# Optimization experiments

Hardware: AMD Instinct MI355X
Metric: run time of the kernel (lower is better)

The kernel has to match this reference:

```python
import jax, jax.numpy as jnp
import numpy as np

IN_NC = 32
OUT_NC = 32
EXPAND = 2
HID = IN_NC * EXPAND          # 64
K = 3                         # depthwise kernel
EPS = 1e-5
R1 = IN_NC * HID              # end of pointwise-1 weights
R2 = R1 + HID * K * K         # end of depthwise weights
R3 = R2 + HID * OUT_NC        # total hyper params = 4672


def _bn(t, g, b):
    # BatchNorm2d in training mode over the flattened (b*fh*fw) batch:
    # stats over all axes except the channel axis (axis=3 of [b,fh,fw,C,H,W]).
    ax = (0, 1, 2, 4, 5)
    m = jnp.mean(t, axis=ax, keepdims=True)
    v = jnp.mean((t - m) ** 2, axis=ax, keepdims=True)
    sh = (1, 1, 1, -1, 1, 1)
    return (t - m) * jax.lax.rsqrt(v + EPS) * g.reshape(sh) + b.reshape(sh)


def _relu6(t):
    return jnp.clip(t, 0.0, 6.0)


def setup_inputs() -> dict:
    key = jax.random.key(0)
    k0, k1 = jax.random.split(key)
    x = jax.random.normal(k0, (8, IN_NC, 256, 256), dtype=jnp.float32)
    s = jax.random.normal(k1, (8, R3, 32, 32), dtype=jnp.float32) * 0.1
    return {
        'x': x,
        's': s,
        'gamma1': jnp.ones((HID,), jnp.float32),
        'beta1': jnp.zeros((HID,), jnp.float32),
        'gamma2': jnp.ones((HID,), jnp.float32),
        'beta2': jnp.zeros((HID,), jnp.float32),
        'gamma3': jnp.ones((OUT_NC,), jnp.float32),
        'beta3': jnp.zeros((OUT_NC,), jnp.float32),
    }


def reference(x, s, gamma1, beta1, gamma2, beta2, gamma3, beta3):
    b, c, h, w = x.shape
    fh, fw = s.shape[-2], s.shape[-1]
    ph, pw = h // fh, w // fw          # patch size
    kh, kw = ph + 2, pw + 2            # patch + reflect halo of 1

    # reflect-pad then extract overlapping [kh,kw] patches on a [ph,pw] grid
    xp = jnp.pad(x, ((0, 0), (0, 0), (1, 1), (1, 1)), mode='reflect')
    ri = (jnp.arange(fh) * ph)[:, None] + jnp.arange(kh)   # [fh,kh]
    ci = (jnp.arange(fw) * pw)[:, None] + jnp.arange(kw)   # [fw,kw]
    patches = xp[:, :, ri][:, :, :, :, ci]                 # [b,c,fh,kh,fw,kw]
    patches = patches.transpose(0, 2, 4, 1, 3, 5)          # [b,fh,fw,c,kh,kw]

    sw = s.transpose(0, 2, 3, 1)                           # [b,fh,fw,R3]

    # stage 1: per-patch 1x1 expand conv (in_nc -> hidden)
    w1 = sw[..., :R1].reshape(b, fh, fw, HID, c)
    y = jnp.einsum('bfgoc,bfgchw->bfgohw', w1, patches)    # [b,fh,fw,HID,kh,kw]
    y = _relu6(_bn(y, gamma1, beta1))

    # stage 2: per-patch depthwise 3x3 conv (valid), stride 1 -> [ph,pw]
    w2 = sw[..., R1:R2].reshape(b, fh, fw, HID, K, K)
    z = jnp.zeros((b, fh, fw, HID, ph, pw), y.dtype)
    for u in range(K):
        for v in range(K):
            z = z + w2[..., u, v, None, None] * y[..., u:u + ph, v:v + pw]
    z = _relu6(_bn(z, gamma2, beta2))

    # stage 3: per-patch 1x1 project conv (hidden -> out_nc)
    w3 = sw[..., R2:R3].reshape(b, fh, fw, OUT_NC, HID)
    o = jnp.einsum('bfgoc,bfgcpq->bfgopq', w3, z)          # [b,fh,fw,OUT_NC,ph,pw]
    o = _bn(o, gamma3, beta3)

    # reassemble patches: [b,fh,fw,C,ph,pw] -> [b,C,h,w]
    o = o.transpose(0, 3, 1, 4, 2, 5).reshape(b, OUT_NC, h, w)
    return x + o  # use_res_connect: stride==1 and in_nc==out_nc
```

## Files before the change

kernel.cpp:

```cpp
#include <hip/hip_runtime.h>

#define NT 256

constexpr int R1c = 2048;
constexpr int R2c = 2624;
constexpr float EPSc = 1e-5f;

constexpr int SLOTS1  = 0;
constexpr int SLOTS1Q = 4096;
constexpr int SLOTS2  = 8192;
constexpr int SLOTS2Q = 12288;
constexpr int SLOTS3  = 16384;
constexpr int SLOTS3Q = 18432;
constexpr int STATS_ZERO_FLOATS = 20480;

constexpr size_t ST2_OFF   = 131072;
constexpr size_t ST2_BYTES = 8ull * 1024 * 4672 * 2;
constexpr size_t ZB_OFF    = ST2_OFF + ST2_BYTES;
constexpr size_t ZB_BYTES  = 8192ull * 4096 * 2;
constexpr size_t Y_OFF     = ZB_OFF + ZB_BYTES;
constexpr size_t Y_BYTES   = 8192ull * 13312;
constexpr size_t NEED_Y    = Y_OFF + Y_BYTES;
constexpr size_t OI_OFF    = Y_OFF;

__device__ __forceinline__ ushort f_to_bf16(float f) {
    union { float f; unsigned int i; } v; v.f = f;
    unsigned int r = (v.i + 0x7fffu + ((v.i >> 16) & 1u)) >> 16;
    return (ushort)r;
}
__device__ __forceinline__ float bf16_to_f(ushort u) {
    union { unsigned int i; float f; } v; v.i = ((unsigned int)u) << 16; return v.f;
}
__device__ __forceinline__ float bf16lo_to_f(unsigned int u) {
    union { unsigned int i; float f; } v; v.i = u << 16; return v.f;
}
__device__ __forceinline__ float bf16hi_to_f(unsigned int u) {
    union { unsigned int i; float f; } v; v.i = u & 0xffff0000u; return v.f;
}
__device__ __forceinline__ unsigned int pack_bf16(float lo, float hi) {
    return (unsigned int)f_to_bf16(lo) | ((unsigned int)f_to_bf16(hi) << 16);
}

typedef short bf16x8 __attribute__((ext_vector_type(8)));
typedef float f32x4  __attribute__((ext_vector_type(4)));
union FR { uint4 u4; bf16x8 v; ushort s[8]; };

__device__ __forceinline__ f32x4 mfma16(bf16x8 a, bf16x8 b, f32x4 c) {
    return __builtin_amdgcn_mfma_f32_16x16x32_bf16(a, b, c, 0, 0, 0);
}

__device__ __forceinline__ void dev_fin(const float* __restrict__ ws, int so, int sq,
        const float* __restrict__ gamma, const float* __restrict__ beta,
        int nch, float N, float* finL, int t) {
    if (t < nch) {
        float sm = 0.f, qq = 0.f;
        for (int j = 0; j < 64; j++) { sm += ws[so + t*64 + j]; qq += ws[sq + t*64 + j]; }
        float mean = sm / N;
        float var  = qq / N - mean * mean;
        float a = rsqrtf(var + EPSc) * gamma[t];
        finL[t]       = a;
        finL[nch + t] = beta[t] - mean * a;
    }
    __syncthreads();
}

__global__ __launch_bounds__(256)
void transpose_w(const float* __restrict__ s, ushort* __restrict__ st,
                 float* __restrict__ ws) {
    __shared__ float tl[2112];
    const int tile = blockIdx.x, t = threadIdx.x;
    if (tile < 80) {
        int idx = tile * 256 + t;
        if (idx < STATS_ZERO_FLOATS) ws[idx] = 0.f;
    }
    const int bi = tile / (73 * 32);
    int rem = tile - bi * 73 * 32;
    const int qy = rem / 73, px = rem - qy * 73;
    const int p0 = px * 64, q0 = qy * 32;
    const int tx = t & 31, ty = t >> 5;
    const float* sb = s + (size_t)bi * 4672 * 1024;
    #pragma unroll
    for (int r = ty; r < 64; r += 8)
        tl[r * 33 + tx] = sb[(size_t)(p0 + r) * 1024 + q0 + tx];
    __syncthreads();
    unsigned int* stu = (unsigned int*)(st + (size_t)bi * 1024 * 4672);
    #pragma unroll
    for (int rr = ty; rr < 32; rr += 8) {
        int q = q0 + rr;
        stu[((size_t)q * 4672 + p0) / 2 + tx] =
            pack_bf16(tl[(2 * tx) * 33 + rr], tl[(2 * tx + 1) * 33 + rr]);
    }
}

__global__ __launch_bounds__(NT, 4)
void k1_w(const float* __restrict__ x, const ushort* __restrict__ st2,
          ushort* __restrict__ ybuf, float* __restrict__ ws) {
    __shared__ __align__(16) ushort frB[2 * 3584];
    __shared__ float st1[128];
    const int t = threadIdx.x, unit = blockIdx.x;
    const int bi = unit >> 9, f = (unit >> 4) & 31, jb = unit & 15;
    const int g0 = jb * 2, slot = unit & 63;
    const int w = t >> 6, l = t & 63, l15 = l & 15, grp = l >> 4;
    const int pl_ = w >> 1, mh = w & 1;
    const int patch = bi * 1024 + f * 32 + g0 + pl_;

    if (t < 128) {
        st1[t] = 0.f;
        int p = t >> 6, e = t & 63;
        if ((e & 15) >= 4)
            ((uint4*)frB)[p * 448 + 384 + e] = make_uint4(0u, 0u, 0u, 0u);
    }
    const ushort* wp = st2 + (size_t)patch * 4672;
    FR aw[2];
    #pragma unroll
    for (int i = 0; i < 2; i++)
        aw[i].u4 = ((const uint4*)wp)[((mh * 2 + i) * 16 + l15) * 4 + grp];

    const float* xb = x + (size_t)bi * 32 * 65536;
    for (int i = t; i < 1920; i += NT) {
        int c = i / 60, rem = i - c * 60;
        int r = rem / 6, seg = rem - r * 6;
        int row = f * 8 - 1 + r; row = row < 0 ? -row : (row > 255 ? 510 - row : row);
        int col0 = g0 * 8 - 4 + seg * 4;
        float v4[4];
        if (col0 >= 0 && col0 <= 252) {
            float4 vv = *(const float4*)(xb + (size_t)c * 65536 + row * 256 + col0);
            v4[0] = vv.x; v4[1] = vv.y; v4[2] = vv.z; v4[3] = vv.w;
        } else {
            #pragma unroll
            for (int d = 0; d < 4; d++) {
                int cc = col0 + d; cc = cc < 0 ? -cc : (cc > 255 ? 510 - cc : cc);
                v4[d] = xb[(size_t)c * 65536 + row * 256 + cc];
            }
        }
        int grpc = c >> 3, j = c & 7;
        #pragma unroll
        for (int d = 0; d < 4; d++) {
            int u = col0 + d - g0 * 8;
            ushort hv = f_to_bf16(v4[d]);
            #pragma unroll
            for (int p = 0; p < 2; p++) {
                int pc = u - 8 * p + 1;
                if (pc >= 0 && pc <= 9) {
                    int px = r * 10 + pc;
                    frB[p * 3584 + ((px >> 4) * 64 + grpc * 16 + (px & 15)) * 8 + j] = hv;
                }
            }
        }
    }
    __syncthreads();

    FR b[7];
    const uint4* bp = (const uint4*)(frB + pl_ * 3584);
    #pragma unroll
    for (int n = 0; n < 7; n++) b[n].u4 = bp[n * 64 + l];
    __syncthreads();

    ushort* slice = frB + pl_ * 3584 + mh * 1792;
    unsigned int* sliceU = (unsigned int*)slice;
    uint4* yb4 = (uint4*)ybuf + (size_t)patch * 832;
    float s4[8], q4[8];
    #pragma unroll
    for (int i = 0; i < 8; i++) { s4[i] = 0.f; q4[i] = 0.f; }
    #pragma unroll
    for (int i = 0; i < 2; i++) {
        int mm = mh * 2 + i;
        #pragma unroll
        for (int n = 0; n < 7; n++) {
            f32x4 z = {0.f, 0.f, 0.f, 0.f};
            f32x4 c = mfma16(aw[i].v, b[n].v, z);
            int px = n * 16 + l15;
            #pragma unroll
            for (int r = 0; r < 4; r++) {
                float v = c[r]; s4[i*4+r] += v; q4[i*4+r] += v * v;
                if (px < 100) slice[(grp * 4 + r) * 106 + px] = f_to_bf16(v);
            }
        }
        for (int k = l; k < 208; k += 64) {
            int ch2 = k / 13, sub = k - ch2 * 13;
            int ub = ch2 * 53 + sub * 4;
            yb4[mm * 208 + k] = make_uint4(sliceU[ub], sliceU[ub+1], sliceU[ub+2], sliceU[ub+3]);
        }
    }
    #pragma unroll
    for (int i = 0; i < 8; i++) {
        float sm = s4[i], qq = q4[i];
        #pragma unroll
        for (int msk = 1; msk <= 8; msk <<= 1) { sm += __shfl_xor(sm, msk); qq += __shfl_xor(qq, msk); }
        if (l15 == 0) {
            int ch = (mh * 2 + (i >> 2)) * 16 + grp * 4 + (i & 3);
            atomicAdd(&st1[ch], sm);
            atomicAdd(&st1[64 + ch], qq);
        }
    }
    __syncthreads();
    if (t < 64) {
        atomicAdd(&ws[SLOTS1  + t * 64 + slot], st1[t]);
        atomicAdd(&ws[SLOTS1Q + t * 64 + slot], st1[64 + t]);
    }
}

__global__ __launch_bounds__(NT, 4)
void k2_w(const ushort* __restrict__ ybuf, const ushort* __restrict__ st2,
          ushort* __restrict__ zbuf, float* __restrict__ ws,
          const float* __restrict__ g1, const float* __restrict__ b1) {
    __shared__ __align__(16) ushort slc[4 * 1696];
    __shared__ unsigned int w2L[2 * 288];
    __shared__ float finL[128];
    __shared__ float accL[128];
    const int t = threadIdx.x, unit = blockIdx.x;
    const int bi = unit >> 9, f = (unit >> 4) & 31, jb = unit & 15;
    const int g0 = jb * 2, slot = unit & 63;
    const int w = t >> 6, l = t & 63;
    const int pl_ = w >> 1, mh = w & 1;
    const int ch_l = l >> 2, quad = l & 3, p0 = quad * 2;
    const int patch = bi * 1024 + f * 32 + g0 + pl_;

    dev_fin(ws, SLOTS1, SLOTS1Q, g1, b1, 64, 819200.0f, finL, t);
    if (t < 128) accL[t] = 0.f;
    for (int k = t; k < 576; k += NT) {
        int p = (k >= 288) ? 1 : 0;
        int kk = k - p * 288;
        const unsigned int* src = (const unsigned int*)(st2 + (size_t)(bi*1024 + f*32 + g0 + p) * 4672 + R1c);
        w2L[k] = src[kk];
    }
    __syncthreads();

    const uint4* yb4 = (const uint4*)ybuf + (size_t)patch * 832;
    ushort* slice = slc + w * 1696;
    unsigned int* sliceU = (unsigned int*)slice;
    const ushort* w2u = (const ushort*)(w2L + pl_ * 288);
    ushort* zp0 = zbuf + (size_t)patch * 4096;

    #pragma unroll
    for (int i = 0; i < 2; i++) {
        int mm = mh * 2 + i;
        for (int k = l; k < 208; k += 64) {
            uint4 v = yb4[mm * 208 + k];
            int ch2 = k / 13, sub = k - ch2 * 13;
            int ch = mm * 16 + ch2;
            float a1 = finL[ch], bb1 = finL[64 + ch];
            unsigned int uu[4] = {v.x, v.y, v.z, v.w};
            int ub = ch2 * 53 + sub * 4;
            #pragma unroll
            for (int kk = 0; kk < 4; kk++) {
                float lo = fminf(fmaxf(bf16lo_to_f(uu[kk]) * a1 + bb1, 0.f), 6.f);
                float hi = fminf(fmaxf(bf16hi_to_f(uu[kk]) * a1 + bb1, 0.f), 6.f);
                sliceU[ub + kk] = pack_bf16(lo, hi);
            }
        }
        float yv[4][10];
        #pragma unroll
        for (int rr = 0; rr < 4; rr++) {
            int base = ch_l * 53 + (p0 + rr) * 5;
            #pragma unroll
            for (int k = 0; k < 5; k++) {
                unsigned int u = sliceU[base + k];
                yv[rr][2*k] = bf16lo_to_f(u); yv[rr][2*k+1] = bf16hi_to_f(u);
            }
        }
        float wt[9];
        #pragma unroll
        for (int k = 0; k < 9; k++) wt[k] = bf16_to_f(w2u[(mm * 16 + ch_l) * 9 + k]);
        float za[2][8];
        #pragma unroll
        for (int rr = 0; rr < 2; rr++)
            #pragma unroll
            for (int q = 0; q < 8; q++) za[rr][q] = 0.f;
        #pragma unroll
        for (int u = 0; u < 3; u++)
            #pragma unroll
            for (int v = 0; v < 3; v++) {
                float wv = wt[u * 3 + v];
                #pragma unroll
                for (int rr = 0; rr < 2; rr++)
                    #pragma unroll
                    for (int q = 0; q < 8; q++)
                        za[rr][q] += wv * yv[rr + u][q + v];
            }
        float zs = 0.f, zq = 0.f;
        #pragma unroll
        for (int rr = 0; rr < 2; rr++)
            #pragma unroll
            for (int q = 0; q < 8; q++) { float v = za[rr][q]; zs += v; zq += v * v; }
        zs += __shfl_xor(zs, 1); zs += __shfl_xor(zs, 2);
        zq += __shfl_xor(zq, 1); zq += __shfl_xor(zq, 2);
        if (quad == 0) {
            atomicAdd(&accL[mm * 16 + ch_l], zs);
            atomicAdd(&accL[64 + mm * 16 + ch_l], zq);
        }
        ushort* zp = zp0 + (mm * 16 + ch_l) * 64 + p0 * 8;
        uint4 pk0, pk1;
        pk0.x = pack_bf16(za[0][0], za[0][1]); pk0.y = pack_bf16(za[0][2], za[0][3]);
        pk0.z = pack_bf16(za[0][4], za[0][5]); pk0.w = pack_bf16(za[0][6], za[0][7]);
        pk1.x = pack_bf16(za[1][0], za[1][1]); pk1.y = pack_bf16(za[1][2], za[1][3]);
        pk1.z = pack_bf16(za[1][4], za[1][5]); pk1.w = pack_bf16(za[1][6], za[1][7]);
        *(uint4*)zp = pk0;
        *(uint4*)(zp + 8) = pk1;
    }
    __syncthreads();
    if (t < 64) {
        atomicAdd(&ws[SLOTS2  + t * 64 + slot], accL[t]);
        atomicAdd(&ws[SLOTS2Q + t * 64 + slot], accL[64 + t]);
    }
}

__global__ __launch_bounds__(NT, 4)
void k3_w(const ushort* __restrict__ zbuf, const ushort* __restrict__ st2,
          ushort* __restrict__ oi, float* __restrict__ ws,
          const float* __restrict__ g2, const float* __restrict__ b2) {
    __shared__ __align__(16) ushort zL[2 * 4224];
    __shared__ float finL[128];
    __shared__ float accL[64];
    const int t = threadIdx.x, unit = blockIdx.x;
    const int bi = unit >> 9, f = (unit >> 4) & 31, jb = unit & 15;
    const int g0 = jb * 2, slot = unit & 63;
    const int w = t >> 6, l = t & 63, l15 = l & 15, grp = l >> 4;
    const int pl_ = w >> 1, mh = w & 1;
    const int patch = bi * 1024 + f * 32 + g0 + pl_;

    dev_fin(ws, SLOTS2, SLOTS2Q, g2, b2, 64, 524288.0f, finL, t);
    if (t < 64) accL[t] = 0.f;
    const ushort* wp = st2 + (size_t)patch * 4672;
    FR aw[2];
    #pragma unroll
    for (int ks = 0; ks < 2; ks++)
        aw[ks].u4 = ((const uint4*)(wp + R2c))[(mh * 16 + l15) * 8 + ks * 4 + grp];

    const uint4* zsrc = (const uint4*)(zbuf + (size_t)patch * 4096);
    unsigned int* zd = (unsigned int*)zL;
    #pragma unroll
    for (int it = 0; it < 4; it++) {
        int i = mh * 256 + it * 64 + l;
        uint4 v = zsrc[i];
        int ch = i >> 3, px0 = (i & 7) * 8;
        float a2 = finL[ch], bb2 = finL[64 + ch];
        unsigned int uu[4] = {v.x, v.y, v.z, v.w};
        int base = pl_ * 2112 + (ch * 66 + px0) / 2;
        #pragma unroll
        for (int k = 0; k < 4; k++) {
            float lo = fminf(fmaxf(bf16lo_to_f(uu[k]) * a2 + bb2, 0.f), 6.f);
            float hi = fminf(fmaxf(bf16hi_to_f(uu[k]) * a2 + bb2, 0.f), 6.f);
            zd[base + k] = pack_bf16(lo, hi);
        }
    }
    __syncthreads();

    FR bfr[2][4];
    #pragma unroll
    for (int ks = 0; ks < 2; ks++)
        #pragma unroll
        for (int n = 0; n < 4; n++)
            #pragma unroll
            for (int j = 0; j < 8; j++)
                bfr[ks][n].s[j] = zL[pl_ * 4224 + (ks * 32 + grp * 8 + j) * 66 + n * 16 + l15];

    float s4[4], q4[4];
    #pragma unroll
    for (int r = 0; r < 4; r++) { s4[r] = 0.f; q4[r] = 0.f; }
    #pragma unroll
    for (int n = 0; n < 4; n++) {
        f32x4 z = {0.f, 0.f, 0.f, 0.f};
        f32x4 c = mfma16(aw[0].v, bfr[0][n].v, z);
        c = mfma16(aw[1].v, bfr[1][n].v, c);
        #pragma unroll
        for (int r = 0; r < 4; r++) {
            float v = c[r];
            s4[r] += v; q4[r] += v * v;
            int oc = mh * 16 + grp * 4 + r;
            int px = n * 16 + l15, p = px >> 3, q = px & 7;
            oi[((size_t)(bi * 32 + oc) * 256 + f * 8 + p) * 256 + (g0 + pl_) * 8 + q] = f_to_bf16(v);
        }
    }
    #pragma unroll
    for (int r = 0; r < 4; r++) {
        float sm = s4[r], qq = q4[r];
        #pragma unroll
        for (int msk = 1; msk <= 8; msk <<= 1) { sm += __shfl_xor(sm, msk); qq += __shfl_xor(qq, msk); }
        if (l15 == 0) {
            int oc = mh * 16 + grp * 4 + r;
            atomicAdd(&accL[oc], sm);
            atomicAdd(&accL[32 + oc], qq);
        }
    }
    __syncthreads();
    if (t < 32) {
        atomicAdd(&ws[SLOTS3  + t * 64 + slot], accL[t]);
        atomicAdd(&ws[SLOTS3Q + t * 64 + slot], accL[32 + t]);
    }
}

__global__ __launch_bounds__(NT, 8)
void k4_w(const float* __restrict__ x, float* __restrict__ ws,
          const ushort* __restrict__ oi, float* __restrict__ out,
          const float* __restrict__ g3, const float* __restrict__ b3) {
    __shared__ float finL[64];
    dev_fin(ws, SLOTS3, SLOTS3Q, g3, b3, 32, 524288.0f, finL, threadIdx.x);
    #pragma unroll
    for (int it = 0; it < 8; it++) {
        size_t e = ((size_t)(it * 2048 + blockIdx.x) * 256 + threadIdx.x) * 4;
        int oc = (int)((e >> 16) & 31);
        float a3 = finL[oc], bb3 = finL[32 + oc];
        uint2 ov = *(const uint2*)(oi + e);
        float4 xv = *(const float4*)(x + e);
        float4 r;
        r.x = xv.x + bf16lo_to_f(ov.x) * a3 + bb3;
        r.y = xv.y + bf16hi_to_f(ov.x) * a3 + bb3;
        r.z = xv.z + bf16lo_to_f(ov.y) * a3 + bb3;
        r.w = xv.w + bf16hi_to_f(ov.y) * a3 + bb3;
        *(float4*)(out + e) = r;
    }
}

extern "C" void kernel_launch(void* const* d_in, const int* in_sizes, int n_in,
                              void* d_out, int out_size, void* d_ws, size_t ws_size,
                              hipStream_t stream) {
    const float* x  = (const float*)d_in[0];
    const float* s  = (const float*)d_in[1];
    const float* g1 = (const float*)d_in[2];
    const float* b1 = (const float*)d_in[3];
    const float* g2 = (const float*)d_in[4];
    const float* b2 = (const float*)d_in[5];
    const float* g3 = (const float*)d_in[6];
    const float* b3 = (const float*)d_in[7];
    float* out = (float*)d_out;
    float* ws  = (float*)d_ws;

    ushort* st2 = (ushort*)((char*)d_ws + ST2_OFF);
    ushort* zb  = (ushort*)((char*)d_ws + ZB_OFF);
    ushort* yb  = (ushort*)((char*)d_ws + Y_OFF);
    ushort* oi  = (ushort*)((char*)d_ws + OI_OFF);

    transpose_w<<<18688, 256, 0, stream>>>(s, st2, ws);
    k1_w<<<4096, NT, 0, stream>>>(x, st2, yb, ws);
    k2_w<<<4096, NT, 0, stream>>>(yb, st2, zb, ws, g1, b1);
    k3_w<<<4096, NT, 0, stream>>>(zb, st2, oi, ws, g2, b2);
    k4_w<<<2048, NT, 0, stream>>>(x, ws, oi, out, g3, b3);
}
```

Before: 288.2 us.

## Split weight transpose across k1 and k2 to overlap with compute

The standalone transpose of the hypernetwork weights is split into three parts. The first kernel transposes only the pointwise-1 columns (tiles 0-31). Extra blocks appended to k1 transpose the depthwise columns, and extra blocks appended to k2 transpose the project-weight columns, so the memory-bound transpose can overlap with the compute kernels. The final residual store also becomes nontemporal. In exchange, k1 and k2 get heterogeneous block roles, and correctness relies on the needed slices being written before the kernels that read them.

New measurement: 268.9 us. 6.7% less time.

```diff
diff --git a/kernel.cpp b/kernel.cpp
--- a/kernel.cpp
+++ b/kernel.cpp
@@ -43,6 +43,7 @@
 
 typedef short bf16x8 __attribute__((ext_vector_type(8)));
 typedef float f32x4  __attribute__((ext_vector_type(4)));
+typedef float f32x4n __attribute__((ext_vector_type(4)));
 union FR { uint4 u4; bf16x8 v; ushort s[8]; };
 
 __device__ __forceinline__ f32x4 mfma16(bf16x8 a, bf16x8 b, f32x4 c) {
@@ -64,19 +65,8 @@
     __syncthreads();
 }
 
-__global__ __launch_bounds__(256)
-void transpose_w(const float* __restrict__ s, ushort* __restrict__ st,
-                 float* __restrict__ ws) {
-    __shared__ float tl[2112];
-    const int tile = blockIdx.x, t = threadIdx.x;
-    if (tile < 80) {
-        int idx = tile * 256 + t;
-        if (idx < STATS_ZERO_FLOATS) ws[idx] = 0.f;
-    }
-    const int bi = tile / (73 * 32);
-    int rem = tile - bi * 73 * 32;
-    const int qy = rem / 73, px = rem - qy * 73;
-    const int p0 = px * 64, q0 = qy * 32;
+__device__ __forceinline__ void tr_tile(int bi, int p0, int q0, int t,
+        const float* __restrict__ s, ushort* __restrict__ st, float* tl) {
     const int tx = t & 31, ty = t >> 5;
     const float* sb = s + (size_t)bi * 4672 * 1024;
     #pragma unroll
@@ -92,12 +82,36 @@
     }
 }
 
+__global__ __launch_bounds__(256)
+void transpose_w1(const float* __restrict__ s, ushort* __restrict__ st,
+                  float* __restrict__ ws) {
+    __shared__ float tl[2112];
+    const int blk = blockIdx.x, t = threadIdx.x;
+    if (blk < 80) {
+        int idx = blk * 256 + t;
+        if (idx < STATS_ZERO_FLOATS) ws[idx] = 0.f;
+    }
+    const int bi = blk >> 10, rem = blk & 1023;
+    const int qy = rem >> 5, px = rem & 31;
+    tr_tile(bi, px * 64, qy * 32, t, s, st, tl);
+}
+
 __global__ __launch_bounds__(NT, 4)
-void k1_w(const float* __restrict__ x, const ushort* __restrict__ st2,
-          ushort* __restrict__ ybuf, float* __restrict__ ws) {
+void k1_w(const float* __restrict__ x, const float* __restrict__ s,
+          ushort* __restrict__ st2, ushort* __restrict__ ybuf,
+          float* __restrict__ ws) {
     __shared__ __align__(16) ushort frB[2 * 3584];
     __shared__ float st1[128];
     const int t = threadIdx.x, unit = blockIdx.x;
+
+    if (unit >= 4096) {
+        int u = unit - 4096;
+        int bi = u / 288, rem = u - bi * 288;
+        int qy = rem / 9, px = 32 + (rem - qy * 9);
+        tr_tile(bi, px * 64, qy * 32, t, s, st2, (float*)frB);
+        return;
+    }
+
     const int bi = unit >> 9, f = (unit >> 4) & 31, jb = unit & 15;
     const int g0 = jb * 2, slot = unit & 63;
     const int w = t >> 6, l = t & 63, l15 = l & 15, grp = l >> 4;
@@ -201,14 +215,24 @@
 }
 
 __global__ __launch_bounds__(NT, 4)
-void k2_w(const ushort* __restrict__ ybuf, const ushort* __restrict__ st2,
-          ushort* __restrict__ zbuf, float* __restrict__ ws,
+void k2_w(const ushort* __restrict__ ybuf, const float* __restrict__ s,
+          ushort* __restrict__ st2, ushort* __restrict__ zbuf,
+          float* __restrict__ ws,
           const float* __restrict__ g1, const float* __restrict__ b1) {
     __shared__ __align__(16) ushort slc[4 * 1696];
     __shared__ unsigned int w2L[2 * 288];
     __shared__ float finL[128];
     __shared__ float accL[128];
     const int t = threadIdx.x, unit = blockIdx.x;
+
+    if (unit >= 4096) {
+        int u = unit - 4096;
+        int bi = u >> 10, rem = u & 1023;
+        int qy = rem >> 5, px = 41 + (rem & 31);
+        tr_tile(bi, px * 64, qy * 32, t, s, st2, (float*)slc);
+        return;
+    }
+
     const int bi = unit >> 9, f = (unit >> 4) & 31, jb = unit & 15;
     const int g0 = jb * 2, slot = unit & 63;
     const int w = t >> 6, l = t & 63;
@@ -403,12 +427,12 @@
         float a3 = finL[oc], bb3 = finL[32 + oc];
         uint2 ov = *(const uint2*)(oi + e);
         float4 xv = *(const float4*)(x + e);
-        float4 r;
+        f32x4n r;
         r.x = xv.x + bf16lo_to_f(ov.x) * a3 + bb3;
         r.y = xv.y + bf16hi_to_f(ov.x) * a3 + bb3;
         r.z = xv.z + bf16lo_to_f(ov.y) * a3 + bb3;
         r.w = xv.w + bf16hi_to_f(ov.y) * a3 + bb3;
-        *(float4*)(out + e) = r;
+        __builtin_nontemporal_store(r, (f32x4n*)(out + e));
     }
 }
 
@@ -431,9 +455,9 @@
     ushort* yb  = (ushort*)((char*)d_ws + Y_OFF);
     ushort* oi  = (ushort*)((char*)d_ws + OI_OFF);
 
-    transpose_w<<<18688, 256, 0, stream>>>(s, st2, ws);
-    k1_w<<<4096, NT, 0, stream>>>(x, st2, yb, ws);
-    k2_w<<<4096, NT, 0, stream>>>(yb, st2, zb, ws, g1, b1);
+    transpose_w1<<<8192, 256, 0, stream>>>(s, st2, ws);
+    k1_w<<<6400, NT, 0, stream>>>(x, s, st2, yb, ws);
+    k2_w<<<12288, NT, 0, stream>>>(yb, s, st2, zb, ws, g1, b1);
     k3_w<<<4096, NT, 0, stream>>>(zb, st2, oi, ws, g2, b2);
     k4_w<<<2048, NT, 0, stream>>>(x, ws, oi, out, g3, b3);
 }
```
